# Performance work log

Hardware: AMD Instinct MI355X
Metric: run time of the kernel (lower is better)

## Reference

```python
import jax, jax.numpy as jnp
import numpy as np

T, H, I = 4096, 4096, 11008  # tokens, hidden, intermediate


def setup_inputs() -> dict:
    key = jax.random.key(0)
    k = jax.random.split(key, 6)
    # int8-range quantized activations and weights (stored as int32 for jax matmul)
    x_q = jax.random.randint(k[0], (T, H), -127, 128).astype(jnp.int32)
    w_gate_up = jax.random.randint(k[1], (2 * I, H), -127, 128).astype(jnp.int32)
    w_down = jax.random.randint(k[2], (H, I), -127, 128).astype(jnp.int32)
    # per-token dynamic input scale, per-output-channel weight scales
    x_scale = jax.random.uniform(k[3], (T,), jnp.float32, 1e-4, 2e-2)
    s_w_gate_up = jax.random.uniform(k[4], (2 * I,), jnp.float32, 1e-4, 2e-2)
    s_w_down = jax.random.uniform(k[5], (H,), jnp.float32, 1e-4, 2e-2)
    return {"x_q": x_q, "x_scale": x_scale, "w_gate_up": w_gate_up,
            "s_w_gate_up": s_w_gate_up, "w_down": w_down, "s_w_down": s_w_down}


def reference(x_q, x_scale, w_gate_up, s_w_gate_up, w_down, s_w_down):
    # --- gate_up_proj: W8A8 int8 GEMM + dequant (per-token x per-channel scales) ---
    gu_i32 = jnp.matmul(x_q, w_gate_up.T)                                   # [T, 2I] int32 accum
    gu = gu_i32.astype(jnp.float32) * x_scale[:, None] * s_w_gate_up[None, :]
    gate, up = gu[:, :I], gu[:, I:]
    # --- SiluAndMulQuant: fused SiLU(gate)*up + per-token dynamic requant to int8 ---
    y = jax.nn.silu(gate) * up                                              # [T, I] fp
    s2 = jnp.maximum(jnp.max(jnp.abs(y), axis=-1), 1e-8) / 127.0            # [T] new dynamic scale
    y_q = jnp.clip(jnp.round(y / s2[:, None]), -128.0, 127.0).astype(jnp.int32)
    # --- down_proj: W8A8 int8 GEMM + dequant ---
    out_i32 = jnp.matmul(y_q, w_down.T)                                     # [T, H] int32 accum
    out = out_i32.astype(jnp.float32) * s2[:, None] * s_w_down[None, :]
    return out
```

## Files before the change

kernel.cpp:

```cpp
#include <hip/hip_runtime.h>
#include <cstdint>
#include <cstddef>

#define T_DIM 4096
#define H_DIM 4096
#define I_DIM 11008

typedef int v4i __attribute__((ext_vector_type(4)));

__device__ __forceinline__ void async_copy16(const void* g, void* l) {
  __builtin_amdgcn_global_load_lds(
      (const __attribute__((address_space(1))) void*)g,
      (__attribute__((address_space(3))) void*)l, 16, 0, 0);
}

__device__ __forceinline__ void stage_tile(const int8_t* src, size_t ld,
                                           char* ldsbase, int wave, int lane) {
#pragma unroll
  for (int q = 0; q < 2; ++q) {
    int seg = q * 4 + wave;
    int r = seg * 16 + (lane >> 2);
    int p = lane & 3;
    int c = p ^ ((r >> 1) & 3);
    const int8_t* g = src + (size_t)r * ld + (size_t)c * 16;
    char* lp = ldsbase + seg * 1024;
    async_copy16((const void*)g, (void*)lp);
  }
}

__device__ __forceinline__ v4i frag_load(const char* ldsbase, int rowbase, int lane) {
  int r = rowbase + (lane & 15);
  int c = (lane >> 4) ^ ((r >> 1) & 3);
  return *(const v4i*)(ldsbase + r * 64 + c * 16);
}

__global__ void pack_i8(const int4* __restrict__ src, char4* __restrict__ dst, int n4) {
  int stride = gridDim.x * blockDim.x;
  for (int i = blockIdx.x * blockDim.x + threadIdx.x; i < n4; i += stride) {
    int4 v = src[i];
    char4 c;
    c.x = (char)v.x; c.y = (char)v.y; c.z = (char)v.z; c.w = (char)v.w;
    dst[i] = c;
  }
}

__global__ void zero_u32(unsigned* __restrict__ p, int n) {
  int i = blockIdx.x * blockDim.x + threadIdx.x;
  if (i < n) p[i] = 0u;
}

__device__ __forceinline__ void g1_step(const char* LA, const char* LBG, const char* LBU,
                                        int wm, int wn, int lane,
                                        v4i (&accg)[4][4], v4i (&accu)[4][4]) {
  v4i a[4], bg[4], bu[4];
#pragma unroll
  for (int i = 0; i < 4; i++) a[i]  = frag_load(LA,  wm * 64 + i * 16, lane);
#pragma unroll
  for (int j = 0; j < 4; j++) bg[j] = frag_load(LBG, wn * 64 + j * 16, lane);
#pragma unroll
  for (int j = 0; j < 4; j++) bu[j] = frag_load(LBU, wn * 64 + j * 16, lane);
#pragma unroll
  for (int i = 0; i < 4; i++)
#pragma unroll
    for (int j = 0; j < 4; j++) {
      accg[i][j] = __builtin_amdgcn_mfma_i32_16x16x64_i8(a[i], bg[j], accg[i][j], 0, 0, 0);
      accu[i][j] = __builtin_amdgcn_mfma_i32_16x16x64_i8(a[i], bu[j], accu[i][j], 0, 0, 0);
    }
}

__global__ __launch_bounds__(256, 2)
void gemm1_silu(const int8_t* __restrict__ x8,
                const int8_t* __restrict__ wgu8,
                const float* __restrict__ x_scale,
                const float* __restrict__ s_wgu,
                float* __restrict__ y,
                unsigned* __restrict__ rowmax) {
  __shared__ __align__(16) char lds0[24576];
  __shared__ __align__(16) char lds1[24576];
  char* A0 = lds0;  char* Bg0 = lds0 + 8192;  char* Bu0 = lds0 + 16384;
  char* A1 = lds1;  char* Bg1 = lds1 + 8192;  char* Bu1 = lds1 + 16384;

  const int tid = threadIdx.x;
  const int wave = tid >> 6, lane = tid & 63;
  const int wm = wave >> 1, wn = wave & 1;

  const unsigned nwg = gridDim.x * gridDim.y;
  const unsigned bid = blockIdx.y * gridDim.x + blockIdx.x;
  const unsigned cpx = nwg >> 3;
  const unsigned swz = (bid & 7) * cpx + (bid >> 3);
  const int m0 = (int)(swz / gridDim.x) * 128;
  const int n0 = (int)(swz % gridDim.x) * 128;

  v4i accg[4][4], accu[4][4];
  const v4i vzero = {0, 0, 0, 0};
#pragma unroll
  for (int i = 0; i < 4; i++)
#pragma unroll
    for (int j = 0; j < 4; j++) { accg[i][j] = vzero; accu[i][j] = vzero; }

  const int8_t* Ab  = x8 + (size_t)m0 * H_DIM;
  const int8_t* Bgb = wgu8 + (size_t)n0 * H_DIM;
  const int8_t* Bub = wgu8 + ((size_t)I_DIM + (size_t)n0) * H_DIM;

  stage_tile(Ab,  H_DIM, A0,  wave, lane);
  stage_tile(Bgb, H_DIM, Bg0, wave, lane);
  stage_tile(Bub, H_DIM, Bu0, wave, lane);
  __syncthreads();

  for (int k0 = 0; k0 < H_DIM; k0 += 128) {
    {
      const int kn = k0 + 64;
      if (kn < H_DIM) {
        stage_tile(Ab + kn,  H_DIM, A1,  wave, lane);
        stage_tile(Bgb + kn, H_DIM, Bg1, wave, lane);
        stage_tile(Bub + kn, H_DIM, Bu1, wave, lane);
      }
      g1_step(A0, Bg0, Bu0, wm, wn, lane, accg, accu);
      __syncthreads();
    }
    {
      const int kn = k0 + 128;
      if (kn < H_DIM) {
        stage_tile(Ab + kn,  H_DIM, A0,  wave, lane);
        stage_tile(Bgb + kn, H_DIM, Bg0, wave, lane);
        stage_tile(Bub + kn, H_DIM, Bu0, wave, lane);
      }
      g1_step(A1, Bg1, Bu1, wm, wn, lane, accg, accu);
      __syncthreads();
    }
  }

  const int lr = lane >> 4;
  const int lc = lane & 15;
#pragma unroll
  for (int i = 0; i < 4; i++) {
#pragma unroll
    for (int t = 0; t < 4; t++) {
      const int gr = m0 + wm * 64 + i * 16 + lr * 4 + t;
      const float sx = x_scale[gr];
      float vmax = 0.f;
#pragma unroll
      for (int j = 0; j < 4; j++) {
        const int gc = n0 + wn * 64 + j * 16 + lc;
        float g = (float)accg[i][j][t] * sx * s_wgu[gc];
        float u = (float)accu[i][j][t] * sx * s_wgu[I_DIM + gc];
        float yv = (g / (1.f + expf(-g))) * u;
        y[(size_t)gr * I_DIM + gc] = yv;
        vmax = fmaxf(vmax, fabsf(yv));
      }
#pragma unroll
      for (int off = 1; off < 16; off <<= 1)
        vmax = fmaxf(vmax, __shfl_xor(vmax, off, 64));
      if (lc == 0) atomicMax(&rowmax[gr], __float_as_uint(vmax));
    }
  }
}

__global__ void quantize_y(const float* __restrict__ y,
                           const unsigned* __restrict__ rowmax,
                           int8_t* __restrict__ yq) {
  size_t gid = (size_t)blockIdx.x * blockDim.x + threadIdx.x;
  size_t base = gid * 4;
  if (base >= (size_t)T_DIM * I_DIM) return;
  int row = (int)(base / I_DIM);
  float inv = 127.f / fmaxf(__uint_as_float(rowmax[row]), 1e-8f);
  float4 v = *(const float4*)(y + base);
  char4 q;
  q.x = (char)(int)fminf(127.f, fmaxf(-128.f, rintf(v.x * inv)));
  q.y = (char)(int)fminf(127.f, fmaxf(-128.f, rintf(v.y * inv)));
  q.z = (char)(int)fminf(127.f, fmaxf(-128.f, rintf(v.z * inv)));
  q.w = (char)(int)fminf(127.f, fmaxf(-128.f, rintf(v.w * inv)));
  *(char4*)(yq + base) = q;
}

__device__ __forceinline__ void g2_step(const char* LA, const char* LB,
                                        int wm, int wn, int lane,
                                        v4i (&acc)[4][4]) {
  v4i a[4], b[4];
#pragma unroll
  for (int i = 0; i < 4; i++) a[i] = frag_load(LA, wm * 64 + i * 16, lane);
#pragma unroll
  for (int j = 0; j < 4; j++) b[j] = frag_load(LB, wn * 64 + j * 16, lane);
#pragma unroll
  for (int i = 0; i < 4; i++)
#pragma unroll
    for (int j = 0; j < 4; j++)
      acc[i][j] = __builtin_amdgcn_mfma_i32_16x16x64_i8(a[i], b[j], acc[i][j], 0, 0, 0);
}

__global__ __launch_bounds__(256, 3)
void gemm2_scaled(const int8_t* __restrict__ yq8,
                  const int8_t* __restrict__ wd8,
                  const unsigned* __restrict__ rowmax,
                  const float* __restrict__ s_wd,
                  float* __restrict__ out) {
  __shared__ __align__(16) char lds0[16384];
  __shared__ __align__(16) char lds1[16384];
  char* A0 = lds0;  char* B0 = lds0 + 8192;
  char* A1 = lds1;  char* B1 = lds1 + 8192;

  const int tid = threadIdx.x;
  const int wave = tid >> 6, lane = tid & 63;
  const int wm = wave >> 1, wn = wave & 1;

  const unsigned nwg = gridDim.x * gridDim.y;
  const unsigned bid = blockIdx.y * gridDim.x + blockIdx.x;
  const unsigned cpx = nwg >> 3;
  const unsigned swz = (bid & 7) * cpx + (bid >> 3);
  const int m0 = (int)(swz / gridDim.x) * 128;
  const int n0 = (int)(swz % gridDim.x) * 128;

  v4i acc[4][4];
  const v4i vzero = {0, 0, 0, 0};
#pragma unroll
  for (int i = 0; i < 4; i++)
#pragma unroll
    for (int j = 0; j < 4; j++) acc[i][j] = vzero;

  const int8_t* Ab = yq8 + (size_t)m0 * I_DIM;
  const int8_t* Bb = wd8 + (size_t)n0 * I_DIM;

  stage_tile(Ab, I_DIM, A0, wave, lane);
  stage_tile(Bb, I_DIM, B0, wave, lane);
  __syncthreads();

  for (int k0 = 0; k0 < I_DIM; k0 += 128) {
    {
      const int kn = k0 + 64;
      if (kn < I_DIM) {
        stage_tile(Ab + kn, I_DIM, A1, wave, lane);
        stage_tile(Bb + kn, I_DIM, B1, wave, lane);
      }
      g2_step(A0, B0, wm, wn, lane, acc);
      __syncthreads();
    }
    {
      const int kn = k0 + 128;
      if (kn < I_DIM) {
        stage_tile(Ab + kn, I_DIM, A0, wave, lane);
        stage_tile(Bb + kn, I_DIM, B0, wave, lane);
      }
      g2_step(A1, B1, wm, wn, lane, acc);
      __syncthreads();
    }
  }

  const int lr = lane >> 4;
  const int lc = lane & 15;
#pragma unroll
  for (int i = 0; i < 4; i++) {
#pragma unroll
    for (int t = 0; t < 4; t++) {
      const int gr = m0 + wm * 64 + i * 16 + lr * 4 + t;
      const float s2 = fmaxf(__uint_as_float(rowmax[gr]), 1e-8f) / 127.f;
#pragma unroll
      for (int j = 0; j < 4; j++) {
        const int gc = n0 + wn * 64 + j * 16 + lc;
        out[(size_t)gr * H_DIM + gc] = (float)acc[i][j][t] * s2 * s_wd[gc];
      }
    }
  }
}

extern "C" void kernel_launch(void* const* d_in, const int* in_sizes, int n_in,
                              void* d_out, int out_size, void* d_ws, size_t ws_size,
                              hipStream_t stream) {
  const int*   x_q     = (const int*)d_in[0];
  const float* x_scale = (const float*)d_in[1];
  const int*   w_gu    = (const int*)d_in[2];
  const float* s_wgu   = (const float*)d_in[3];
  const int*   w_d     = (const int*)d_in[4];
  const float* s_wd    = (const float*)d_in[5];
  float* out = (float*)d_out;

  char* ws = (char*)d_ws;
  const size_t SZ_X8   = (size_t)T_DIM * H_DIM;
  const size_t SZ_WGU8 = (size_t)2 * I_DIM * H_DIM;
  const size_t SZ_WD8  = (size_t)H_DIM * I_DIM;
  const size_t SZ_Y    = (size_t)T_DIM * I_DIM * 4;
  const size_t SZ_YQ   = (size_t)T_DIM * I_DIM;

  int8_t*   x8     = (int8_t*)ws;
  int8_t*   wgu8   = (int8_t*)(ws + SZ_X8);
  int8_t*   wd8    = (int8_t*)(ws + SZ_X8 + SZ_WGU8);
  float*    y      = (float*)(ws + SZ_X8 + SZ_WGU8 + SZ_WD8);
  int8_t*   yq8    = (int8_t*)(ws + SZ_X8 + SZ_WGU8 + SZ_WD8 + SZ_Y);
  unsigned* rowmax = (unsigned*)(ws + SZ_X8 + SZ_WGU8 + SZ_WD8 + SZ_Y + SZ_YQ);

  pack_i8<<<dim3(8192), dim3(256), 0, stream>>>((const int4*)x_q,  (char4*)x8,   (int)(SZ_X8 / 4));
  pack_i8<<<dim3(8192), dim3(256), 0, stream>>>((const int4*)w_gu, (char4*)wgu8, (int)(SZ_WGU8 / 4));
  pack_i8<<<dim3(8192), dim3(256), 0, stream>>>((const int4*)w_d,  (char4*)wd8,  (int)(SZ_WD8 / 4));
  zero_u32<<<dim3(16), dim3(256), 0, stream>>>(rowmax, T_DIM);

  gemm1_silu<<<dim3(I_DIM / 128, T_DIM / 128), dim3(256), 0, stream>>>(
      x8, wgu8, x_scale, s_wgu, y, rowmax);

  quantize_y<<<dim3((unsigned)((size_t)T_DIM * I_DIM / 4 / 256)), dim3(256), 0, stream>>>(
      y, rowmax, yq8);

  gemm2_scaled<<<dim3(H_DIM / 128, T_DIM / 128), dim3(256), 0, stream>>>(
      yq8, wd8, rowmax, s_wd, out);
}
```

Baseline: 1.475 ms.

## Triple-buffer LDS in both int8 GEMMs with two-stage-deep async prefetch

Both GEMM kernels move from a double-buffered LDS ring to a three-buffer ring. Global-to-LDS loads are issued two K-steps ahead. Each step now uses one explicit s_waitcnt on vmcnt plus a single barrier, replacing the trailing __syncthreads, so more memory latency can overlap with MFMA work. The cost is 50% more LDS per workgroup: 72KB for gemm1 and 48KB for gemm2. That reduces the headroom for the requested occupancy and relies on hand-counted vmcnt values matching the loads issued by stage_tile.

```diff
diff --git a/kernel.cpp b/kernel.cpp
--- a/kernel.cpp
+++ b/kernel.cpp
@@ -77,8 +77,10 @@
                 unsigned* __restrict__ rowmax) {
   __shared__ __align__(16) char lds0[24576];
   __shared__ __align__(16) char lds1[24576];
-  char* A0 = lds0;  char* Bg0 = lds0 + 8192;  char* Bu0 = lds0 + 16384;
-  char* A1 = lds1;  char* Bg1 = lds1 + 8192;  char* Bu1 = lds1 + 16384;
+  __shared__ __align__(16) char lds2[24576];
+  char* Abuf[3]  = {lds0,         lds1,         lds2};
+  char* Bgbuf[3] = {lds0 + 8192,  lds1 + 8192,  lds2 + 8192};
+  char* Bubuf[3] = {lds0 + 16384, lds1 + 16384, lds2 + 16384};
 
   const int tid = threadIdx.x;
   const int wave = tid >> 6, lane = tid & 63;
@@ -102,33 +104,37 @@
   const int8_t* Bgb = wgu8 + (size_t)n0 * H_DIM;
   const int8_t* Bub = wgu8 + ((size_t)I_DIM + (size_t)n0) * H_DIM;
 
-  stage_tile(Ab,  H_DIM, A0,  wave, lane);
-  stage_tile(Bgb, H_DIM, Bg0, wave, lane);
-  stage_tile(Bub, H_DIM, Bu0, wave, lane);
-  __syncthreads();
-
-  for (int k0 = 0; k0 < H_DIM; k0 += 128) {
-    {
-      const int kn = k0 + 64;
-      if (kn < H_DIM) {
-        stage_tile(Ab + kn,  H_DIM, A1,  wave, lane);
-        stage_tile(Bgb + kn, H_DIM, Bg1, wave, lane);
-        stage_tile(Bub + kn, H_DIM, Bu1, wave, lane);
-      }
-      g1_step(A0, Bg0, Bu0, wm, wn, lane, accg, accu);
-      __syncthreads();
-    }
-    {
-      const int kn = k0 + 128;
-      if (kn < H_DIM) {
-        stage_tile(Ab + kn,  H_DIM, A0,  wave, lane);
-        stage_tile(Bgb + kn, H_DIM, Bg0, wave, lane);
-        stage_tile(Bub + kn, H_DIM, Bu0, wave, lane);
-      }
-      g1_step(A1, Bg1, Bu1, wm, wn, lane, accg, accu);
-      __syncthreads();
-    }
-  }
+  stage_tile(Ab,       H_DIM, Abuf[0],  wave, lane);
+  stage_tile(Bgb,      H_DIM, Bgbuf[0], wave, lane);
+  stage_tile(Bub,      H_DIM, Bubuf[0], wave, lane);
+  stage_tile(Ab + 64,  H_DIM, Abuf[1],  wave, lane);
+  stage_tile(Bgb + 64, H_DIM, Bgbuf[1], wave, lane);
+  stage_tile(Bub + 64, H_DIM, Bubuf[1], wave, lane);
+
+#define G1_PHASE(B, T)                                                    \
+  {                                                                       \
+    asm volatile("s_waitcnt vmcnt(6) lgkmcnt(0)" ::: "memory");           \
+    __builtin_amdgcn_s_barrier();                                         \
+    __builtin_amdgcn_sched_barrier(0);                                    \
+    const int kn_ = ((T) + 2) << 6;                                       \
+    if (kn_ < H_DIM) {                                                    \
+      stage_tile(Ab + kn_,  H_DIM, Abuf[((B) + 2) % 3],  wave, lane);     \
+      stage_tile(Bgb + kn_, H_DIM, Bgbuf[((B) + 2) % 3], wave, lane);     \
+      stage_tile(Bub + kn_, H_DIM, Bubuf[((B) + 2) % 3], wave, lane);     \
+    }                                                                     \
+    g1_step(Abuf[(B)], Bgbuf[(B)], Bubuf[(B)], wm, wn, lane, accg, accu); \
+  }
+
+  for (int t = 0; t < 63; t += 3) {
+    G1_PHASE(0, t)
+    G1_PHASE(1, t + 1)
+    G1_PHASE(2, t + 2)
+  }
+  asm volatile("s_waitcnt vmcnt(0) lgkmcnt(0)" ::: "memory");
+  __builtin_amdgcn_s_barrier();
+  __builtin_amdgcn_sched_barrier(0);
+  g1_step(Abuf[0], Bgbuf[0], Bubuf[0], wm, wn, lane, accg, accu);
+#undef G1_PHASE
 
   const int lr = lane >> 4;
   const int lc = lane & 15;
@@ -196,8 +202,9 @@
                   float* __restrict__ out) {
   __shared__ __align__(16) char lds0[16384];
   __shared__ __align__(16) char lds1[16384];
-  char* A0 = lds0;  char* B0 = lds0 + 8192;
-  char* A1 = lds1;  char* B1 = lds1 + 8192;
+  __shared__ __align__(16) char lds2[16384];
+  char* Abuf[3] = {lds0,        lds1,        lds2};
+  char* Bbuf[3] = {lds0 + 8192, lds1 + 8192, lds2 + 8192};
 
   const int tid = threadIdx.x;
   const int wave = tid >> 6, lane = tid & 63;
@@ -220,30 +227,34 @@
   const int8_t* Ab = yq8 + (size_t)m0 * I_DIM;
   const int8_t* Bb = wd8 + (size_t)n0 * I_DIM;
 
-  stage_tile(Ab, I_DIM, A0, wave, lane);
-  stage_tile(Bb, I_DIM, B0, wave, lane);
-  __syncthreads();
-
-  for (int k0 = 0; k0 < I_DIM; k0 += 128) {
-    {
-      const int kn = k0 + 64;
-      if (kn < I_DIM) {
-        stage_tile(Ab + kn, I_DIM, A1, wave, lane);
-        stage_tile(Bb + kn, I_DIM, B1, wave, lane);
-      }
-      g2_step(A0, B0, wm, wn, lane, acc);
-      __syncthreads();
-    }
-    {
-      const int kn = k0 + 128;
-      if (kn < I_DIM) {
-        stage_tile(Ab + kn, I_DIM, A0, wave, lane);
-        stage_tile(Bb + kn, I_DIM, B0, wave, lane);
-      }
-      g2_step(A1, B1, wm, wn, lane, acc);
-      __syncthreads();
-    }
-  }
+  stage_tile(Ab,      I_DIM, Abuf[0], wave, lane);
+  stage_tile(Bb,      I_DIM, Bbuf[0], wave, lane);
+  stage_tile(Ab + 64, I_DIM, Abuf[1], wave, lane);
+  stage_tile(Bb + 64, I_DIM, Bbuf[1], wave, lane);
+
+#define G2_PHASE(B, T)                                                    \
+  {                                                                       \
+    asm volatile("s_waitcnt vmcnt(4) lgkmcnt(0)" ::: "memory");           \
+    __builtin_amdgcn_s_barrier();                                         \
+    __builtin_amdgcn_sched_barrier(0);                                    \
+    const int kn_ = ((T) + 2) << 6;                                       \
+    if (kn_ < I_DIM) {                                                    \
+      stage_tile(Ab + kn_, I_DIM, Abuf[((B) + 2) % 3], wave, lane);       \
+      stage_tile(Bb + kn_, I_DIM, Bbuf[((B) + 2) % 3], wave, lane);       \
+    }                                                                     \
+    g2_step(Abuf[(B)], Bbuf[(B)], wm, wn, lane, acc);                     \
+  }
+
+  for (int t = 0; t < 171; t += 3) {
+    G2_PHASE(0, t)
+    G2_PHASE(1, t + 1)
+    G2_PHASE(2, t + 2)
+  }
+  asm volatile("s_waitcnt vmcnt(0) lgkmcnt(0)" ::: "memory");
+  __builtin_amdgcn_s_barrier();
+  __builtin_amdgcn_sched_barrier(0);
+  g2_step(Abuf[0], Bbuf[0], wm, wn, lane, acc);
+#undef G2_PHASE
 
   const int lr = lane >> 4;
   const int lc = lane & 15;
```

Measured after the change: 1.729 ms. +17.2%, slower.
